# Kernel optimization log

Measured on AMD Instinct MI355X. Metric: run time of the kernel, lower is better.

Reference implementation:

```python
import jax, jax.numpy as jnp
import numpy as np

EPS = 1e-5  # BatchNorm2d default eps


def _bn(x, gamma, beta, mean, var):
    # inference-mode BN over channel dim (NCHW)
    inv = gamma / jnp.sqrt(var + EPS)
    return x * inv[None, :, None, None] + (beta - mean * inv)[None, :, None, None]


def _shift(x):
    # 4 channel groups shifted by 1 pixel in 4 directions, zero-fill at borders
    C = x.shape[1]
    gc = C // 4
    g0, g1, g2, g3 = (x[:, i * gc:(i + 1) * gc] for i in range(4))
    g0 = jnp.pad(g0[:, :, :, :-1], ((0, 0), (0, 0), (0, 0), (1, 0)))  # shift right (W)
    g1 = jnp.pad(g1[:, :, 1:, :], ((0, 0), (0, 0), (0, 1), (0, 0)))   # shift up (H)
    g2 = jnp.pad(g2[:, :, :, 1:], ((0, 0), (0, 0), (0, 0), (0, 1)))   # shift left (W)
    g3 = jnp.pad(g3[:, :, :-1, :], ((0, 0), (0, 0), (1, 0), (0, 0)))  # shift down (H)
    return jnp.concatenate([g0, g1, g2, g3], axis=1)


def setup_inputs() -> dict:
    key = jax.random.key(0)
    ks = jax.random.split(key, 8)
    B, C1, C2, H, W = 16, 128, 256, 128, 128
    x = jax.random.normal(ks[0], (B, C1, H, W), dtype=jnp.float32)
    w_conv = jax.random.normal(ks[1], (C2, C1, 3, 3), dtype=jnp.float32) * (1.0 / np.sqrt(C1 * 9))
    w_1x1 = jax.random.normal(ks[2], (C2, C2, 1, 1), dtype=jnp.float32) * (1.0 / np.sqrt(C2))
    b_1x1 = jax.random.normal(ks[3], (C2,), dtype=jnp.float32) * 0.05
    gamma = jax.random.uniform(ks[4], (C2,), dtype=jnp.float32, minval=0.5, maxval=1.5)
    beta = jax.random.normal(ks[5], (C2,), dtype=jnp.float32) * 0.1
    bn_mean = jax.random.normal(ks[6], (C2,), dtype=jnp.float32) * 0.1
    bn_var = jax.random.uniform(ks[7], (C2,), dtype=jnp.float32, minval=0.5, maxval=1.5)
    return {"x": x, "w_conv": w_conv, "w_1x1": w_1x1, "b_1x1": b_1x1,
            "gamma": gamma, "beta": beta, "bn_mean": bn_mean, "bn_var": bn_var}


def reference(x, w_conv, w_1x1, b_1x1, gamma, beta, bn_mean, bn_var):
    # conv3x3 (stride 1, 'same' via autopad=1, no bias) + BN + SiLU
    y = jax.lax.conv_general_dilated(
        x, w_conv, window_strides=(1, 1), padding=((1, 1), (1, 1)),
        dimension_numbers=("NCHW", "OIHW", "NCHW"))
    y = jax.nn.silu(_bn(y, gamma, beta, bn_mean, bn_var))
    identity = y
    # shift + conv1x1 (with bias) + same BN + residual + SiLU
    z = _shift(y)
    z = jax.lax.conv_general_dilated(
        z, w_1x1, window_strides=(1, 1), padding=((0, 0), (0, 0)),
        dimension_numbers=("NCHW", "OIHW", "NCHW")) + b_1x1[None, :, None, None]
    z = _bn(z, gamma, beta, bn_mean, bn_var) + identity
    return jax.nn.silu(z)
```

## Files before the change

### kernel.cpp

```cpp
#include <hip/hip_runtime.h>

typedef unsigned short u16;
typedef unsigned int   u32;
typedef __bf16 bf16x8 __attribute__((ext_vector_type(8)));
typedef float  f32x4  __attribute__((ext_vector_type(4)));

__device__ __forceinline__ float bf2f(u16 v){ u32 u = ((u32)v) << 16; float f; __builtin_memcpy(&f,&u,4); return f; }
__device__ __forceinline__ u16 f2bf(float f){ u32 u; __builtin_memcpy(&u,&f,4); u32 r = (u + 0x7FFFu + ((u>>16)&1u)) >> 16; return (u16)r; }
__device__ __forceinline__ float silu(float v){ return v / (1.f + __expf(-v)); }

__device__ __forceinline__ void gload_lds16(const u16* g, u16* l){
  __builtin_amdgcn_global_load_lds((const __attribute__((address_space(1))) void*)g,
                                   (__attribute__((address_space(3))) void*)l, 16, 0, 0);
}

#define FENCE asm volatile("" ::: "memory")
#define BARRIER do{ FENCE; __builtin_amdgcn_s_barrier(); FENCE; }while(0)

#define HP 130
#define XPIX 128
#define YPIX 256
#define XIMG (HP*HP*XPIX)
#define YIMG (HP*HP*YPIX)

__global__ void prep_coef(const float* __restrict__ gamma, const float* __restrict__ beta,
                          const float* __restrict__ mean,  const float* __restrict__ var,
                          const float* __restrict__ b1, float2* __restrict__ coefA, float2* __restrict__ coefB){
  int c = threadIdx.x;
  float s = gamma[c] * rsqrtf(var[c] + 1e-5f);
  float t = beta[c] - mean[c] * s;
  coefA[c] = make_float2(s, t);
  coefB[c] = make_float2(s, b1[c] * s + t);
}

__global__ void repack_w3(const float* __restrict__ w, u16* __restrict__ w3p){
  int idx = blockIdx.x*256 + threadIdx.x;
  int n = idx / 1152, k = idx % 1152;
  int tap = k >> 7, c = k & 127;
  int kh = tap / 3, kw = tap % 3;
  w3p[idx] = f2bf(w[((n*128 + c)*3 + kh)*3 + kw]);
}

__global__ void repack_w1(const float* __restrict__ w, u16* __restrict__ w1p){
  int idx = blockIdx.x*256 + threadIdx.x;
  w1p[idx] = f2bf(w[idx]);
}

__device__ __forceinline__ void halo_pix(int pi, int& hp, int& wp){
  if (pi < 130){ hp = 0; wp = pi; }
  else if (pi < 260){ hp = 129; wp = pi - 130; }
  else { int j = pi - 260; hp = 1 + (j >> 1); wp = (j & 1) ? 129 : 0; }
}
__global__ void zero_halos(u16* __restrict__ xpad, u16* __restrict__ ypad, int cimg){
  int idx = blockIdx.x*256 + threadIdx.x;
  const int NX = cimg*516*16;
  uint4 z = make_uint4(0u,0u,0u,0u);
  if (idx < NX){
    int b = idx / (516*16), rr = idx % (516*16);
    int pi = rr >> 4, cch = rr & 15, hp, wp;
    halo_pix(pi, hp, wp);
    *(uint4*)(xpad + (((size_t)b*HP + hp)*HP + wp)*XPIX + cch*8) = z;
  } else {
    idx -= NX;
    if (idx < cimg*516*32){
      int b = idx / (516*32), rr = idx % (516*32);
      int pi = rr >> 5, cch = rr & 31, hp, wp;
      halo_pix(pi, hp, wp);
      *(uint4*)(ypad + (((size_t)b*HP + hp)*HP + wp)*YPIX + cch*8) = z;
    }
  }
}

__global__ __launch_bounds__(256) void transpose_x(const float* __restrict__ x, u16* __restrict__ xpad, int b0){
  __shared__ u16 s[64][66];
  const int tid = threadIdx.x, bid = blockIdx.x;
  const int ct = bid & 1, wt = (bid >> 1) & 1, row = bid >> 2;
  const int bl = row >> 7, h = row & 127;
  const int c0 = ct << 6, w0 = wt << 6;
  {
    const int lw = tid & 63, lc4 = tid >> 6;
    const size_t xb = ((size_t)(b0 + bl)*128)*16384 + (size_t)h*128 + w0 + lw;
    #pragma unroll
    for (int r = 0; r < 16; ++r){
      int c = r*4 + lc4;
      s[c][lw] = f2bf(x[xb + (size_t)(c0 + c)*16384]);
    }
  }
  __syncthreads();
  {
    const int lw = tid >> 5, lcp = (tid & 31) << 1;
    const size_t pb = ((size_t)bl*HP + h + 1)*HP;
    #pragma unroll
    for (int r = 0; r < 8; ++r){
      int w = r*8 + lw;
      u32 v = (u32)s[lcp][w] | ((u32)s[lcp+1][w] << 16);
      *(u32*)(xpad + (pb + (w0 + w + 1))*XPIX + c0 + lcp) = v;
    }
  }
}


__device__ __forceinline__ int offA_of(int Ts){
  int tap = Ts >> 1;
  int kh = (tap*11) >> 5;
  int kw = tap - kh*3;
  return kh*(HP*XPIX) + kw*XPIX + ((Ts & 1) << 6);
}

__global__ __launch_bounds__(512, 2) void convA(const u16* __restrict__ xpad, const u16* __restrict__ w3p,
                                                const float2* __restrict__ coefA, u16* __restrict__ ypad,
                                                int BPW){
  __shared__ u16 sA[2][16384];
  __shared__ u16 sB[2][16384];
  const int t = threadIdx.x;
  const int nwg = gridDim.x;
  const int w = (blockIdx.x & 7)*(nwg >> 3) + (blockIdx.x >> 3);
  const int band0 = w * BPW;
  const int bl = band0 >> 6;
  int h0 = (band0 & 63) << 1;
  const int lane = t & 63, wave = t >> 6;
  const int wm = wave & 1, wn = wave >> 1;
  const int quad = lane >> 4, l16 = lane & 15;
  const int lc = t & 7;
  const u16* ximg = xpad + (size_t)bl * XIMG;

  const u16* gA[2][2]; int lA[2][2];
  const u16* gB[2][2]; int lB[2][2];
  #pragma unroll
  for (int ho = 0; ho < 2; ++ho)
    #pragma unroll
    for (int q = 0; q < 2; ++q){
      int r = ((t >> 6) << 4) + (q << 3) + ((t >> 3) & 7);
      int p = (ho << 6) + r + (r & 64);
      gA[ho][q] = ximg + (size_t)((h0 + (p >> 7))*HP + (p & 127))*XPIX + ((lc ^ (p & 7)) << 3);
      lA[ho][q] = p*64 + lc*8;
      int n = ((r >> 5) << 6) + (ho << 5) + (r & 31);
      gB[ho][q] = w3p + (size_t)n*1152 + ((lc ^ (n & 7)) << 3);
      lB[ho][q] = n*64 + lc*8;
    }

  u32 fA[2][4][2], fB[4][2];
  #pragma unroll
  for (int hf = 0; hf < 2; ++hf)
    #pragma unroll
    for (int i = 0; i < 4; ++i)
      #pragma unroll
      for (int c = 0; c < 2; ++c){
        int row = wm*128 + hf*64 + i*16 + l16;
        fA[hf][i][c] = row*64 + (((c*4 + quad) ^ (row & 7)) << 3);
      }
  #pragma unroll
  for (int j = 0; j < 4; ++j)
    #pragma unroll
    for (int c = 0; c < 2; ++c){
      int row = wn*64 + j*16 + l16;
      fB[j][c] = row*64 + (((c*4 + quad) ^ (row & 7)) << 3);
    }

  f32x4 acc[8][4];
  #pragma unroll
  for (int i = 0; i < 8; ++i)
    #pragma unroll
    for (int j = 0; j < 4; ++j){ f32x4 z = {0.f,0.f,0.f,0.f}; acc[i][j] = z; }

  {
    gload_lds16(gA[0][0], sA[0] + lA[0][0]); gload_lds16(gA[0][1], sA[0] + lA[0][1]);
    gload_lds16(gB[0][0], sB[0] + lB[0][0]); gload_lds16(gB[0][1], sB[0] + lB[0][1]);
    gload_lds16(gB[1][0], sB[0] + lB[1][0]); gload_lds16(gB[1][1], sB[0] + lB[1][1]);
    gload_lds16(gA[1][0], sA[0] + lA[1][0]); gload_lds16(gA[1][1], sA[0] + lA[1][1]);
    asm volatile("s_waitcnt vmcnt(0)" ::: "memory");
  }
  BARRIER;

  const int UTOT = 18 * BPW;
  int tn = 0;
  for (int u = 0; u < UTOT; ++u){
    const int pr = u & 1;
    const u16* A = sA[pr]; const u16* B = sB[pr];
    u16* An = sA[pr ^ 1]; u16* Bn = sB[pr ^ 1];
    const bool last = (u == UTOT - 1);
    const int ntl = (tn == 17) ? 0 : tn + 1;
    if (tn == 17 && !last){
      #pragma unroll
      for (int ho = 0; ho < 2; ++ho)
        #pragma unroll
        for (int q = 0; q < 2; ++q) gA[ho][q] += 2*HP*XPIX;
    }
    const int aoff = offA_of(ntl), boff = ntl*64;

    bf16x8 a[4][2], b[4][2];
    #pragma unroll
    for (int i = 0; i < 4; ++i){
      a[i][0] = *(const bf16x8*)(A + fA[0][i][0]);
      a[i][1] = *(const bf16x8*)(A + fA[0][i][1]);
    }
    #pragma unroll
    for (int j = 0; j < 4; ++j){
      b[j][0] = *(const bf16x8*)(B + fB[j][0]);
      b[j][1] = *(const bf16x8*)(B + fB[j][1]);
    }
    if (!last){
      gload_lds16(gA[0][0] + aoff, An + lA[0][0]); gload_lds16(gA[0][1] + aoff, An + lA[0][1]);
      gload_lds16(gB[0][0] + boff, Bn + lB[0][0]); gload_lds16(gB[0][1] + boff, Bn + lB[0][1]);
    }
    __builtin_amdgcn_s_setprio(1);
    #pragma unroll
    for (int i = 0; i < 4; ++i)
      #pragma unroll
      for (int j = 0; j < 4; ++j){
        acc[i][j] = __builtin_amdgcn_mfma_f32_16x16x32_bf16(a[i][0], b[j][0], acc[i][j], 0, 0, 0);
        acc[i][j] = __builtin_amdgcn_mfma_f32_16x16x32_bf16(a[i][1], b[j][1], acc[i][j], 0, 0, 0);
      }
    __builtin_amdgcn_s_setprio(0);
    if (last) asm volatile("s_waitcnt vmcnt(0)" ::: "memory");
    else      asm volatile("s_waitcnt vmcnt(4)" ::: "memory");
    BARRIER;

    #pragma unroll
    for (int i = 0; i < 4; ++i){
      a[i][0] = *(const bf16x8*)(A + fA[1][i][0]);
      a[i][1] = *(const bf16x8*)(A + fA[1][i][1]);
    }
    if (!last){
      gload_lds16(gB[1][0] + boff, Bn + lB[1][0]); gload_lds16(gB[1][1] + boff, Bn + lB[1][1]);
      gload_lds16(gA[1][0] + aoff, An + lA[1][0]); gload_lds16(gA[1][1] + aoff, An + lA[1][1]);
    }
    __builtin_amdgcn_s_setprio(1);
    #pragma unroll
    for (int i = 0; i < 4; ++i)
      #pragma unroll
      for (int j = 0; j < 4; ++j){
        acc[4+i][j] = __builtin_amdgcn_mfma_f32_16x16x32_bf16(a[i][0], b[j][0], acc[4+i][j], 0, 0, 0);
        acc[4+i][j] = __builtin_amdgcn_mfma_f32_16x16x32_bf16(a[i][1], b[j][1], acc[4+i][j], 0, 0, 0);
      }
    __builtin_amdgcn_s_setprio(0);
    if (!last) asm volatile("s_waitcnt vmcnt(2)" ::: "memory");
    BARRIER;

    if (tn == 17){
      float2 co[4];
      #pragma unroll
      for (int j = 0; j < 4; ++j) co[j] = coefA[wn*64 + j*16 + l16];
      #pragma unroll
      for (int ig = 0; ig < 8; ++ig){
        const int pb = wm*128 + ig*16 + quad*4;
        #pragma unroll
        for (int r = 0; r < 4; ++r){
          const int p = pb + r;
          const int hh = h0 + (p >> 7), ww = p & 127;
          u16* dst = ypad + ((size_t)(bl*HP + hh + 1)*HP + (ww + 1))*YPIX + wn*64;
          #pragma unroll
          for (int j = 0; j < 4; ++j){
            float v = acc[ig][j][r]*co[j].x + co[j].y;
            dst[j*16 + l16] = f2bf(silu(v));
          }
        }
      }
      asm volatile("s_waitcnt vmcnt(0)" ::: "memory");
      h0 += 2;
      tn = 0;
      #pragma unroll
      for (int i = 0; i < 8; ++i)
        #pragma unroll
        for (int j = 0; j < 4; ++j){ f32x4 z = {0.f,0.f,0.f,0.f}; acc[i][j] = z; }
    } else ++tn;
  }
}

__global__ __launch_bounds__(256, 2) void convB(const u16* __restrict__ ypad, const u16* __restrict__ w1p,
                                                const float2* __restrict__ coefB, float* __restrict__ out, int b0){
  __shared__ u16 sAct[2][8192];
  __shared__ u16 sW[2][8192];
  const int tid = threadIdx.x;
  const int nwg = gridDim.x;
  const int bidl = (blockIdx.x & 7)*(nwg >> 3) + (blockIdx.x >> 3);
  const int nt = bidl & 1, row = bidl >> 1;
  const int bl = row >> 7, h = row & 127;
  const int n0 = nt << 7;
  const int lane = tid & 63, wave = tid >> 6;
  const int wc = wave & 1, wpx = wave >> 1;
  const int quad = lane >> 4, l16 = lane & 15;

  const size_t imgy = (size_t)bl * YIMG;

  const u16* gact[4]; const u16* gwt[4]; int ldst[4];
  #pragma unroll
  for (int l = 0; l < 4; ++l){
    int id = l*256 + tid;
    int p = id >> 3, c = id & 7;
    gact[l] = ypad + imgy + (size_t)(h*HP)*YPIX + (size_t)p*YPIX + ((c ^ (p & 7)) << 3);
    gwt[l]  = w1p + (size_t)(n0 + p)*256 + ((c ^ (p & 7)) << 3);
    ldst[l] = id*8;
  }

  u32 fW[4][2], fAc[4][2];
  #pragma unroll
  for (int i = 0; i < 4; ++i)
    #pragma unroll
    for (int k = 0; k < 2; ++k){
      int rn = wc*64 + i*16 + l16;
      fW[i][k] = rn*64 + (((k*4 + quad) ^ (rn & 7)) << 3);
      int rp = wpx*64 + i*16 + l16;
      fAc[i][k] = rp*64 + (((k*4 + quad) ^ (rp & 7)) << 3);
    }

  f32x4 acc[4][4];
  #pragma unroll
  for (int i = 0; i < 4; ++i)
    #pragma unroll
    for (int j = 0; j < 4; ++j){ f32x4 zz = {0.f,0.f,0.f,0.f}; acc[i][j] = zz; }

  {
    const int aoff = (1*HP + 0)*YPIX + 0;
    #pragma unroll
    for (int l = 0; l < 4; ++l){
      gload_lds16(gact[l] + aoff, sAct[0] + ldst[l]);
      gload_lds16(gwt[l],         sW[0]   + ldst[l]);
    }
    asm volatile("s_waitcnt vmcnt(0)" ::: "memory");
  }
  BARRIER;

  #pragma unroll
  for (int g = 0; g < 4; ++g){
    const int pr = g & 1;
    if (g < 3){
      const int gg = g + 1;
      const int dhp = (gg == 1) ? 2 : ((gg == 3) ? 0 : 1);
      const int dwp = (gg == 0) ? 0 : ((gg == 2) ? 2 : 1);
      const int aoff = (dhp*HP + dwp)*YPIX + gg*64;
      const int woff = gg*64;
      #pragma unroll
      for (int l = 0; l < 4; ++l){
        gload_lds16(gact[l] + aoff, sAct[pr^1] + ldst[l]);
        gload_lds16(gwt[l] + woff,  sW[pr^1]   + ldst[l]);
      }
    }
    bf16x8 wf[4][2], af[4][2];
    #pragma unroll
    for (int i = 0; i < 4; ++i){
      wf[i][0] = *(const bf16x8*)(sW[pr] + fW[i][0]);
      wf[i][1] = *(const bf16x8*)(sW[pr] + fW[i][1]);
      af[i][0] = *(const bf16x8*)(sAct[pr] + fAc[i][0]);
      af[i][1] = *(const bf16x8*)(sAct[pr] + fAc[i][1]);
    }
    __builtin_amdgcn_s_setprio(1);
    #pragma unroll
    for (int i = 0; i < 4; ++i)
      #pragma unroll
      for (int j = 0; j < 4; ++j){
        acc[i][j] = __builtin_amdgcn_mfma_f32_16x16x32_bf16(wf[i][0], af[j][0], acc[i][j], 0, 0, 0);
        acc[i][j] = __builtin_amdgcn_mfma_f32_16x16x32_bf16(wf[i][1], af[j][1], acc[i][j], 0, 0, 0);
      }
    __builtin_amdgcn_s_setprio(0);
    asm volatile("s_waitcnt vmcnt(0)" ::: "memory");
    BARRIER;
  }

  const size_t ybase = ((size_t)(bl*HP + h + 1))*HP*YPIX;
  const size_t obase = (size_t)(b0 + bl)*256*16384 + (size_t)h*128;
  #pragma unroll
  for (int i = 0; i < 4; ++i){
    const int chb = n0 + wc*64 + i*16 + quad*4;
    const float2 c0 = coefB[chb+0], c1 = coefB[chb+1], c2 = coefB[chb+2], c3 = coefB[chb+3];
    float* ob = out + obase + (size_t)chb*16384;
    #pragma unroll
    for (int j = 0; j < 4; ++j){
      const int p = wpx*64 + j*16 + l16;
      const ushort4 rv = *(const ushort4*)&ypad[ybase + (size_t)(p + 1)*YPIX + chb];
      ob[p]             = silu(acc[i][j][0]*c0.x + c0.y + bf2f(rv.x));
      ob[16384 + p]     = silu(acc[i][j][1]*c1.x + c1.y + bf2f(rv.y));
      ob[2*16384 + p]   = silu(acc[i][j][2]*c2.x + c2.y + bf2f(rv.z));
      ob[3*16384 + p]   = silu(acc[i][j][3]*c3.x + c3.y + bf2f(rv.w));
    }
  }
}

extern "C" void kernel_launch(void* const* d_in, const int* in_sizes, int n_in,
                              void* d_out, int out_size, void* d_ws, size_t ws_size,
                              hipStream_t stream){
  const float* x  = (const float*)d_in[0];
  const float* w3 = (const float*)d_in[1];
  const float* w1 = (const float*)d_in[2];
  const float* b1 = (const float*)d_in[3];
  const float* gm = (const float*)d_in[4];
  const float* bt = (const float*)d_in[5];
  const float* mn = (const float*)d_in[6];
  const float* vr = (const float*)d_in[7];
  float* outp = (float*)d_out;

  char* ws = (char*)d_ws;
  float2* coefA = (float2*)ws;
  float2* coefB = coefA + 256;
  u16*    w3p   = (u16*)(ws + 4096);
  u16*    w1p   = (u16*)(ws + 4096 + 589824);
  const size_t fixed = 4096 + 589824 + 131072;
  int cimg = 16;
  while (cimg > 1 && fixed + (size_t)cimg*12979200ull > ws_size) cimg >>= 1;
  u16* xpad = (u16*)(ws + fixed);
  u16* ypad = (u16*)(ws + fixed + (size_t)cimg*4326400ull);

  prep_coef<<<1, 256, 0, stream>>>(gm, bt, mn, vr, b1, coefA, coefB);
  repack_w3<<<1152, 256, 0, stream>>>(w3, w3p);
  repack_w1<<<256, 256, 0, stream>>>(w1, w1p);
  {
    int nthr = cimg*516*48;
    zero_halos<<<(nthr + 255)/256, 256, 0, stream>>>(xpad, ypad, cimg);
  }
  const int bands = 64*cimg;
  const int BPW = (bands >= 1024) ? 4 : (bands >= 512 ? 2 : 1);
  const int nwgA = bands / BPW;
  for (int b0 = 0; b0 < 16; b0 += cimg){
    transpose_x<<<4*128*cimg, 256, 0, stream>>>(x, xpad, b0);
    convA<<<nwgA, 512, 0, stream>>>(xpad, w3p, coefA, ypad, BPW);
    convB<<<2*128*cimg, 256, 0, stream>>>(ypad, w1p, coefB, outp, b0);
  }
}
```

Before: 651.0 us.

## Shrink convA to one-row 128x256 tiles with K=32 steps per workgroup

Replaces the persistent 512-thread convA that handled 256-pixel bands (two rows) across several bands per workgroup with a non-persistent 256-thread kernel. Each workgroup now computes one image row (128 pixels × 256 output channels) over 36 K-steps of 32 channels, using smaller LDS buffers and a simpler single-phase loop that waits and synchronises once per step. This aims at higher occupancy and simpler scheduling. In exchange it gives up the larger tile reuse and the split two-phase overlap, and adds more barriers per unit of work plus repeated weight loads across many more workgroups.

Result: slower. 678.2 us (+4.2%).

```diff
diff --git a/kernel.cpp b/kernel.cpp
--- a/kernel.cpp
+++ b/kernel.cpp
@@ -100,62 +100,43 @@
 }
 
 
-__device__ __forceinline__ int offA_of(int Ts){
-  int tap = Ts >> 1;
+__device__ __forceinline__ int offA_of(int kt){
+  int tap = kt >> 2;
   int kh = (tap*11) >> 5;
   int kw = tap - kh*3;
-  return kh*(HP*XPIX) + kw*XPIX + ((Ts & 1) << 6);
-}
-
-__global__ __launch_bounds__(512, 2) void convA(const u16* __restrict__ xpad, const u16* __restrict__ w3p,
-                                                const float2* __restrict__ coefA, u16* __restrict__ ypad,
-                                                int BPW){
-  __shared__ u16 sA[2][16384];
-  __shared__ u16 sB[2][16384];
+  return kh*(HP*XPIX) + kw*XPIX + ((kt & 3) << 5);
+}
+
+__global__ __launch_bounds__(256, 2) void convA(const u16* __restrict__ xpad, const u16* __restrict__ w3p,
+                                                const float2* __restrict__ coefA, u16* __restrict__ ypad){
+  __shared__ u16 sA[2][4096];
+  __shared__ u16 sB[2][8192];
   const int t = threadIdx.x;
   const int nwg = gridDim.x;
-  const int w = (blockIdx.x & 7)*(nwg >> 3) + (blockIdx.x >> 3);
-  const int band0 = w * BPW;
-  const int bl = band0 >> 6;
-  int h0 = (band0 & 63) << 1;
-  const int lane = t & 63, wave = t >> 6;
-  const int wm = wave & 1, wn = wave >> 1;
+  const int bidl = (blockIdx.x & 7)*(nwg >> 3) + (blockIdx.x >> 3);
+  const int bl = bidl >> 7, h = bidl & 127;
+  const int lane = t & 63, wn = t >> 6;
   const int quad = lane >> 4, l16 = lane & 15;
-  const int lc = t & 7;
   const u16* ximg = xpad + (size_t)bl * XIMG;
 
-  const u16* gA[2][2]; int lA[2][2];
-  const u16* gB[2][2]; int lB[2][2];
-  #pragma unroll
-  for (int ho = 0; ho < 2; ++ho)
-    #pragma unroll
-    for (int q = 0; q < 2; ++q){
-      int r = ((t >> 6) << 4) + (q << 3) + ((t >> 3) & 7);
-      int p = (ho << 6) + r + (r & 64);
-      gA[ho][q] = ximg + (size_t)((h0 + (p >> 7))*HP + (p & 127))*XPIX + ((lc ^ (p & 7)) << 3);
-      lA[ho][q] = p*64 + lc*8;
-      int n = ((r >> 5) << 6) + (ho << 5) + (r & 31);
-      gB[ho][q] = w3p + (size_t)n*1152 + ((lc ^ (n & 7)) << 3);
-      lB[ho][q] = n*64 + lc*8;
-    }
-
-  u32 fA[2][4][2], fB[4][2];
-  #pragma unroll
-  for (int hf = 0; hf < 2; ++hf)
-    #pragma unroll
-    for (int i = 0; i < 4; ++i)
-      #pragma unroll
-      for (int c = 0; c < 2; ++c){
-        int row = wm*128 + hf*64 + i*16 + l16;
-        fA[hf][i][c] = row*64 + (((c*4 + quad) ^ (row & 7)) << 3);
-      }
-  #pragma unroll
-  for (int j = 0; j < 4; ++j)
-    #pragma unroll
-    for (int c = 0; c < 2; ++c){
-      int row = wn*64 + j*16 + l16;
-      fB[j][c] = row*64 + (((c*4 + quad) ^ (row & 7)) << 3);
-    }
+  const u16* gA[2]; int lAo[2];
+  #pragma unroll
+  for (int q = 0; q < 2; ++q){
+    int id = t + q*256, p = id >> 2, c = id & 3, cs = c ^ ((p >> 1) & 3);
+    gA[q] = ximg + (size_t)(h*HP + p)*XPIX + cs*8;
+    lAo[q] = id*8;
+  }
+  const u16* gB[4]; int lBo[4];
+  #pragma unroll
+  for (int q = 0; q < 4; ++q){
+    int id = t + q*256, n = id >> 2, c = id & 3, cs = c ^ ((n >> 1) & 3);
+    gB[q] = w3p + (size_t)n*1152 + cs*8;
+    lBo[q] = id*8;
+  }
+
+  const int xq = (quad ^ ((l16 >> 1) & 3)) << 3;
+  const u32 fAb = (u32)l16*32 + xq;
+  const u32 fBb = (u32)(wn*64 + l16)*32 + xq;
 
   f32x4 acc[8][4];
   #pragma unroll
@@ -164,107 +145,63 @@
     for (int j = 0; j < 4; ++j){ f32x4 z = {0.f,0.f,0.f,0.f}; acc[i][j] = z; }
 
   {
-    gload_lds16(gA[0][0], sA[0] + lA[0][0]); gload_lds16(gA[0][1], sA[0] + lA[0][1]);
-    gload_lds16(gB[0][0], sB[0] + lB[0][0]); gload_lds16(gB[0][1], sB[0] + lB[0][1]);
-    gload_lds16(gB[1][0], sB[0] + lB[1][0]); gload_lds16(gB[1][1], sB[0] + lB[1][1]);
-    gload_lds16(gA[1][0], sA[0] + lA[1][0]); gload_lds16(gA[1][1], sA[0] + lA[1][1]);
+    const int o = offA_of(0);
+    gload_lds16(gA[0] + o, sA[0] + lAo[0]);
+    gload_lds16(gA[1] + o, sA[0] + lAo[1]);
+    #pragma unroll
+    for (int q = 0; q < 4; ++q) gload_lds16(gB[q], sB[0] + lBo[q]);
     asm volatile("s_waitcnt vmcnt(0)" ::: "memory");
   }
   BARRIER;
 
-  const int UTOT = 18 * BPW;
-  int tn = 0;
-  for (int u = 0; u < UTOT; ++u){
-    const int pr = u & 1;
+  for (int kt = 0; kt < 36; ++kt){
+    const int pr = kt & 1;
     const u16* A = sA[pr]; const u16* B = sB[pr];
     u16* An = sA[pr ^ 1]; u16* Bn = sB[pr ^ 1];
-    const bool last = (u == UTOT - 1);
-    const int ntl = (tn == 17) ? 0 : tn + 1;
-    if (tn == 17 && !last){
-      #pragma unroll
-      for (int ho = 0; ho < 2; ++ho)
-        #pragma unroll
-        for (int q = 0; q < 2; ++q) gA[ho][q] += 2*HP*XPIX;
-    }
-    const int aoff = offA_of(ntl), boff = ntl*64;
-
-    bf16x8 a[4][2], b[4][2];
-    #pragma unroll
-    for (int i = 0; i < 4; ++i){
-      a[i][0] = *(const bf16x8*)(A + fA[0][i][0]);
-      a[i][1] = *(const bf16x8*)(A + fA[0][i][1]);
-    }
-    #pragma unroll
-    for (int j = 0; j < 4; ++j){
-      b[j][0] = *(const bf16x8*)(B + fB[j][0]);
-      b[j][1] = *(const bf16x8*)(B + fB[j][1]);
-    }
-    if (!last){
-      gload_lds16(gA[0][0] + aoff, An + lA[0][0]); gload_lds16(gA[0][1] + aoff, An + lA[0][1]);
-      gload_lds16(gB[0][0] + boff, Bn + lB[0][0]); gload_lds16(gB[0][1] + boff, Bn + lB[0][1]);
-    }
+
+    if (kt < 35){
+      const int ao = offA_of(kt + 1), bo = (kt + 1) << 5;
+      gload_lds16(gA[0] + ao, An + lAo[0]);
+      gload_lds16(gA[1] + ao, An + lAo[1]);
+      #pragma unroll
+      for (int q = 0; q < 4; ++q) gload_lds16(gB[q] + bo, Bn + lBo[q]);
+    }
+
+    bf16x8 a[8], b[4];
+    a[0] = *(const bf16x8*)(A + fAb);
+    #pragma unroll
+    for (int j = 0; j < 4; ++j) b[j] = *(const bf16x8*)(B + fBb + j*512);
+    #pragma unroll
+    for (int i = 1; i < 8; ++i) a[i] = *(const bf16x8*)(A + fAb + i*512);
+
     __builtin_amdgcn_s_setprio(1);
     #pragma unroll
-    for (int i = 0; i < 4; ++i)
+    for (int i = 0; i < 8; ++i)
+      #pragma unroll
+      for (int j = 0; j < 4; ++j)
+        acc[i][j] = __builtin_amdgcn_mfma_f32_16x16x32_bf16(a[i], b[j], acc[i][j], 0, 0, 0);
+    __builtin_amdgcn_s_setprio(0);
+
+    asm volatile("s_waitcnt vmcnt(0)" ::: "memory");
+    BARRIER;
+  }
+
+  float2 co[4];
+  #pragma unroll
+  for (int j = 0; j < 4; ++j) co[j] = coefA[wn*64 + j*16 + l16];
+  const size_t ybase = ((size_t)(bl*HP + h + 1))*HP*YPIX;
+  #pragma unroll
+  for (int i = 0; i < 8; ++i)
+    #pragma unroll
+    for (int r = 0; r < 4; ++r){
+      const int p = i*16 + quad*4 + r;
+      u16* dst = ypad + ybase + (size_t)(p + 1)*YPIX + wn*64;
       #pragma unroll
       for (int j = 0; j < 4; ++j){
-        acc[i][j] = __builtin_amdgcn_mfma_f32_16x16x32_bf16(a[i][0], b[j][0], acc[i][j], 0, 0, 0);
-        acc[i][j] = __builtin_amdgcn_mfma_f32_16x16x32_bf16(a[i][1], b[j][1], acc[i][j], 0, 0, 0);
+        float v = acc[i][j][r]*co[j].x + co[j].y;
+        dst[j*16 + l16] = f2bf(silu(v));
       }
-    __builtin_amdgcn_s_setprio(0);
-    if (last) asm volatile("s_waitcnt vmcnt(0)" ::: "memory");
-    else      asm volatile("s_waitcnt vmcnt(4)" ::: "memory");
-    BARRIER;
-
-    #pragma unroll
-    for (int i = 0; i < 4; ++i){
-      a[i][0] = *(const bf16x8*)(A + fA[1][i][0]);
-      a[i][1] = *(const bf16x8*)(A + fA[1][i][1]);
-    }
-    if (!last){
-      gload_lds16(gB[1][0] + boff, Bn + lB[1][0]); gload_lds16(gB[1][1] + boff, Bn + lB[1][1]);
-      gload_lds16(gA[1][0] + aoff, An + lA[1][0]); gload_lds16(gA[1][1] + aoff, An + lA[1][1]);
-    }
-    __builtin_amdgcn_s_setprio(1);
-    #pragma unroll
-    for (int i = 0; i < 4; ++i)
-      #pragma unroll
-      for (int j = 0; j < 4; ++j){
-        acc[4+i][j] = __builtin_amdgcn_mfma_f32_16x16x32_bf16(a[i][0], b[j][0], acc[4+i][j], 0, 0, 0);
-        acc[4+i][j] = __builtin_amdgcn_mfma_f32_16x16x32_bf16(a[i][1], b[j][1], acc[4+i][j], 0, 0, 0);
-      }
-    __builtin_amdgcn_s_setprio(0);
-    if (!last) asm volatile("s_waitcnt vmcnt(2)" ::: "memory");
-    BARRIER;
-
-    if (tn == 17){
-      float2 co[4];
-      #pragma unroll
-      for (int j = 0; j < 4; ++j) co[j] = coefA[wn*64 + j*16 + l16];
-      #pragma unroll
-      for (int ig = 0; ig < 8; ++ig){
-        const int pb = wm*128 + ig*16 + quad*4;
-        #pragma unroll
-        for (int r = 0; r < 4; ++r){
-          const int p = pb + r;
-          const int hh = h0 + (p >> 7), ww = p & 127;
-          u16* dst = ypad + ((size_t)(bl*HP + hh + 1)*HP + (ww + 1))*YPIX + wn*64;
-          #pragma unroll
-          for (int j = 0; j < 4; ++j){
-            float v = acc[ig][j][r]*co[j].x + co[j].y;
-            dst[j*16 + l16] = f2bf(silu(v));
-          }
-        }
-      }
-      asm volatile("s_waitcnt vmcnt(0)" ::: "memory");
-      h0 += 2;
-      tn = 0;
-      #pragma unroll
-      for (int i = 0; i < 8; ++i)
-        #pragma unroll
-        for (int j = 0; j < 4; ++j){ f32x4 z = {0.f,0.f,0.f,0.f}; acc[i][j] = z; }
-    } else ++tn;
-  }
+    }
 }
 
 __global__ __launch_bounds__(256, 2) void convB(const u16* __restrict__ ypad, const u16* __restrict__ w1p,
@@ -407,12 +344,9 @@
     int nthr = cimg*516*48;
     zero_halos<<<(nthr + 255)/256, 256, 0, stream>>>(xpad, ypad, cimg);
   }
-  const int bands = 64*cimg;
-  const int BPW = (bands >= 1024) ? 4 : (bands >= 512 ? 2 : 1);
-  const int nwgA = bands / BPW;
   for (int b0 = 0; b0 < 16; b0 += cimg){
     transpose_x<<<4*128*cimg, 256, 0, stream>>>(x, xpad, b0);
-    convA<<<nwgA, 512, 0, stream>>>(xpad, w3p, coefA, ypad, BPW);
+    convA<<<128*cimg, 256, 0, stream>>>(xpad, w3p, coefA, ypad);
     convB<<<2*128*cimg, 256, 0, stream>>>(ypad, w1p, coefB, outp, b0);
   }
 }
```
